# Optimization experiments

Hardware: AMD Instinct MI355X
Metric: run time of the kernel (lower is better)

The kernel has to match this reference:

```python
import jax, jax.numpy as jnp
import numpy as np

N_NODES = 50000
N_EDGES = 800000
D_IN = 128
D_OUT = 128
HEADS = 2
NEG_SLOPE = 0.2  # PyG GATConv default


def _gat_layer(x, src, dst, W, att_src, att_dst, bias):
    """One PyG-style GATConv with concat=False (mean over heads).
    x: [N, d_in], W: [d_in, H*d_out], att_src/att_dst: [H, d_out], bias: [d_out].
    Edge (j=src -> i=dst); softmax normalized over incoming edges of each dst node.
    """
    n = x.shape[0]
    d_out = att_src.shape[1]
    h = (x @ W).reshape(n, HEADS, d_out)                       # [N, H, D]
    a_s = jnp.einsum('nhd,hd->nh', h, att_src)                 # [N, H]
    a_d = jnp.einsum('nhd,hd->nh', h, att_dst)                 # [N, H]
    e = jax.nn.leaky_relu(a_s[src] + a_d[dst], NEG_SLOPE)      # [E, H]
    # numerically stable segment softmax over dst
    m = jax.ops.segment_max(e, dst, num_segments=n)            # [N, H]
    p = jnp.exp(e - m[dst])                                    # [E, H]
    s = jax.ops.segment_sum(p, dst, num_segments=n)            # [N, H]
    alpha = p / s[dst]                                         # [E, H]
    msg = h[src] * alpha[:, :, None]                           # [E, H, D]
    out = jax.ops.segment_sum(msg, dst, num_segments=n)        # [N, H, D]
    return out.mean(axis=1) + bias                             # concat=False -> mean heads


def setup_inputs() -> dict:
    key = jax.random.key(0)
    ks = jax.random.split(key, 10)
    sc = 0.05
    return {
        'x': jax.random.normal(ks[0], (N_NODES, D_IN), dtype=jnp.float32),
        'edge_index': jax.random.randint(ks[1], (2, N_EDGES), 0, N_NODES, dtype=jnp.int64),
        'W1': jax.random.normal(ks[2], (D_IN, HEADS * D_IN), dtype=jnp.float32) * sc,
        'att_src1': jax.random.normal(ks[3], (HEADS, D_IN), dtype=jnp.float32) * sc,
        'att_dst1': jax.random.normal(ks[4], (HEADS, D_IN), dtype=jnp.float32) * sc,
        'b1': jnp.zeros((D_IN,), dtype=jnp.float32),
        'W2': jax.random.normal(ks[5], (D_IN, HEADS * D_OUT), dtype=jnp.float32) * sc,
        'att_src2': jax.random.normal(ks[6], (HEADS, D_OUT), dtype=jnp.float32) * sc,
        'att_dst2': jax.random.normal(ks[7], (HEADS, D_OUT), dtype=jnp.float32) * sc,
        'b2': jnp.zeros((D_OUT,), dtype=jnp.float32),
    }


def reference(x, edge_index, W1, att_src1, att_dst1, b1, W2, att_src2, att_dst2, b2):
    n = x.shape[0]
    # PyG GATConv adds self-loops by default -> every node has >=1 incoming edge
    loops = jnp.arange(n, dtype=edge_index.dtype)
    src = jnp.concatenate([edge_index[0], loops])
    dst = jnp.concatenate([edge_index[1], loops])
    x = _gat_layer(x, src, dst, W1, att_src1, att_dst1, b1)
    x = _gat_layer(x, src, dst, W2, att_src2, att_dst2, b2)
    return x
```

## Files before the change

### kernel.cpp

```cpp
#include <hip/hip_runtime.h>
#include <hip/hip_bf16.h>

#define D 128
#define NCOLS 256
#define NPB 256
#define CAP 12288
#define P1CHUNK 4096

using f16x8 = __attribute__((ext_vector_type(8))) _Float16;
using f16x2 = __attribute__((ext_vector_type(2))) _Float16;
using f32x4 = __attribute__((ext_vector_type(4))) float;

__device__ inline int edge_val(const void* ei, int is32, long long idx) {
    if (is32) return ((const int*)ei)[idx];
    return (int)(((const long long*)ei)[idx]);
}

__global__ __launch_bounds__(256) void attprep_kernel(
    const float* __restrict__ W1, const float* __restrict__ as1,
    const float* __restrict__ ad1, float* __restrict__ v_s1,
    float* __restrict__ v_d1, _Float16* __restrict__ wT1,
    const float* __restrict__ W2, const float* __restrict__ as2,
    const float* __restrict__ ad2, float* __restrict__ v_s2,
    float* __restrict__ v_d2, _Float16* __restrict__ wT2,
    const void* __restrict__ ei, int* __restrict__ flag, int* __restrict__ gcnt) {
    int tid = threadIdx.x;
    if (blockIdx.x == 34) {
        gcnt[tid] = 0;
        if (tid == 0) *flag = 0;
        __syncthreads();
        const unsigned* u = (const unsigned*)ei;
        if (u[2 * tid + 1] != 0) *flag = 1;
        return;
    }
    int layer = blockIdx.x >= 17;
    int bx = blockIdx.x - (layer ? 17 : 0);
    const float* W = layer ? W2 : W1;
    const float* att_s = layer ? as2 : as1;
    const float* att_d = layer ? ad2 : ad1;
    float* v_s = layer ? v_s2 : v_s1;
    float* v_d = layer ? v_d2 : v_d1;
    _Float16* wT = layer ? wT2 : wT1;
    if (bx == 16) {
        int h = tid >> 7, d = tid & 127;
        const float* wrow = W + d * NCOLS + h * D;
        const float* as = att_s + h * D;
        const float* ad = att_d + h * D;
        float ss = 0.f, sd = 0.f;
        for (int i = 0; i < D; i += 4) {
            float4 wv = *reinterpret_cast<const float4*>(wrow + i);
            float4 av = *reinterpret_cast<const float4*>(as + i);
            float4 dv = *reinterpret_cast<const float4*>(ad + i);
            ss += wv.x * av.x + wv.y * av.y + wv.z * av.z + wv.w * av.w;
            sd += wv.x * dv.x + wv.y * dv.y + wv.z * dv.z + wv.w * dv.w;
        }
        v_s[tid] = ss;
        v_d[tid] = sd;
    } else {
        int base = bx * 2048 + tid * 8;
#pragma unroll
        for (int t = 0; t < 8; t += 4) {
            int f = base + t;
            int kk = f >> 7, i = f & 127;
            int h = kk >> 7, d = kk & 127;
            float4 wv = *reinterpret_cast<const float4*>(W + d * NCOLS + h * D + i);
            wT[(size_t)(i + 0) * NCOLS + kk] = (_Float16)(0.5f * wv.x);
            wT[(size_t)(i + 1) * NCOLS + kk] = (_Float16)(0.5f * wv.y);
            wT[(size_t)(i + 2) * NCOLS + kk] = (_Float16)(0.5f * wv.z);
            wT[(size_t)(i + 3) * NCOLS + kk] = (_Float16)(0.5f * wv.w);
        }
    }
}

__global__ __launch_bounds__(256) void bin_kernel(
    const void* __restrict__ ei, const int* __restrict__ flag,
    unsigned* __restrict__ bins, int* __restrict__ gcnt, int E, int nbuck) {
    __shared__ int cnt[256], cur[256], gb[256];
    int tid = threadIdx.x;
    int base = blockIdx.x * P1CHUNK;
    int m = min(P1CHUNK, E - base);
    int is32 = *flag;
    cnt[tid] = 0; cur[tid] = 0;
    __syncthreads();
    for (int i = tid; i < m; i += 256) {
        int dst = edge_val(ei, is32, (long long)E + base + i);
        atomicAdd(&cnt[dst >> 8], 1);
    }
    __syncthreads();
    if (tid < nbuck && cnt[tid] > 0) gb[tid] = atomicAdd(&gcnt[tid], cnt[tid]);
    else gb[tid] = 0;
    __syncthreads();
    for (int i = tid; i < m; i += 256) {
        int src = edge_val(ei, is32, base + i);
        int dst = edge_val(ei, is32, (long long)E + base + i);
        int b = dst >> 8;
        int pos = gb[b] + atomicAdd(&cur[b], 1);
        if (pos < CAP)
            bins[(size_t)b * CAP + pos] = ((unsigned)(dst & 255) << 16) | (unsigned)src;
    }
}

__global__ __launch_bounds__(256) void build_kernel(
    const unsigned* __restrict__ bins, const int* __restrict__ gcnt,
    int* __restrict__ row_ptr, int* __restrict__ csr_src, int n, int nbuck) {
    __shared__ unsigned items[CAP];
    __shared__ int deg[256], sc[256], cur[256], pref[256];
    int b = blockIdx.x, tid = threadIdx.x;
    int node0 = b * NPB;
    int nn = min(n - node0, NPB);
    int cnt = min(gcnt[b], CAP);
    int t = 0;
    if (tid < b) {
        int lo = tid * NPB, hi = min(n, lo + NPB);
        t = min(gcnt[tid], CAP) + (hi - lo);
    }
    pref[tid] = t;
    const unsigned* src = bins + (size_t)b * CAP;
    for (int i = tid; i < cnt; i += 256) items[i] = src[i];
    deg[tid] = (tid < nn) ? 1 : 0;
    __syncthreads();
#pragma unroll
    for (int off = 128; off >= 1; off >>= 1) {
        if (tid < off) pref[tid] += pref[tid + off];
        __syncthreads();
    }
    int gb = pref[0];
    for (int i = tid; i < cnt; i += 256) atomicAdd(&deg[(items[i] >> 16) & 255], 1);
    __syncthreads();
    int d = deg[tid];
    sc[tid] = d;
    __syncthreads();
#pragma unroll
    for (int off = 1; off < 256; off <<= 1) {
        int u = (tid >= off) ? sc[tid - off] : 0;
        __syncthreads();
        sc[tid] += u;
        __syncthreads();
    }
    int incl = sc[tid];
    int excl = incl - d;
    if (tid < nn) row_ptr[node0 + tid + 1] = gb + incl;
    if (b == 0 && tid == 0) row_ptr[0] = 0;
    cur[tid] = excl + ((tid < nn) ? 1 : 0);
    if (tid < nn) csr_src[gb + excl] = node0 + tid;
    __syncthreads();
    for (int i = tid; i < cnt; i += 256) {
        unsigned it = items[i];
        int p = atomicAdd(&cur[(it >> 16) & 255], 1);
        csr_src[gb + p] = (int)(it & 0xFFFFu);
    }
}

__global__ __launch_bounds__(256) void prep_x_kernel(
    const float* __restrict__ x, const float* __restrict__ v_s,
    const float* __restrict__ v_d, _Float16* __restrict__ xh,
    float* __restrict__ a_s, float* __restrict__ a_d, int n) {
    int lane = threadIdx.x & 63;
    int node = blockIdx.x * 4 + (threadIdx.x >> 6);
    if (node >= n) return;
    float2 xv = *reinterpret_cast<const float2*>(x + (size_t)node * D + 2 * lane);
    f16x2 hx = {(_Float16)xv.x, (_Float16)xv.y};
    *reinterpret_cast<f16x2*>(xh + (size_t)node * D + 2 * lane) = hx;
    float2 vs0 = *reinterpret_cast<const float2*>(v_s + 2 * lane);
    float2 vs1 = *reinterpret_cast<const float2*>(v_s + D + 2 * lane);
    float2 vd0 = *reinterpret_cast<const float2*>(v_d + 2 * lane);
    float2 vd1 = *reinterpret_cast<const float2*>(v_d + D + 2 * lane);
    float s0 = xv.x * vs0.x + xv.y * vs0.y;
    float s1 = xv.x * vs1.x + xv.y * vs1.y;
    float d0 = xv.x * vd0.x + xv.y * vd0.y;
    float d1 = xv.x * vd1.x + xv.y * vd1.y;
#pragma unroll
    for (int off = 1; off < 64; off <<= 1) {
        s0 += __shfl_xor(s0, off, 64);
        s1 += __shfl_xor(s1, off, 64);
        d0 += __shfl_xor(d0, off, 64);
        d1 += __shfl_xor(d1, off, 64);
    }
    if (lane == 0) {
        *reinterpret_cast<float2*>(a_s + (size_t)node * 2) = make_float2(s0, s1);
        *reinterpret_cast<float2*>(a_d + (size_t)node * 2) = make_float2(d0, d1);
    }
}

__global__ __launch_bounds__(256) void aggregate_kernel(
    const _Float16* __restrict__ xh, const float* __restrict__ a_s,
    const float* __restrict__ a_d, const int* __restrict__ row_ptr,
    const int* __restrict__ csr_src, _Float16* __restrict__ aggh, int n) {
    int lane = threadIdx.x & 63;
    int node = blockIdx.x * 4 + (threadIdx.x >> 6);
    if (node >= n) return;
    int beg = row_ptr[node], end = row_ptr[node + 1];
    float2 ad = *reinterpret_cast<const float2*>(a_d + (size_t)node * 2);
    int sub = lane >> 4, cq = lane & 15;
    float s0 = 0.f, s1 = 0.f;
    float acc0[8] = {}, acc1[8] = {};
    const _Float16* xb = xh + 8 * cq;
    for (int chunk = beg; chunk < end; chunk += 64) {
        int cnt = min(64, end - chunk);
        int j_l = 0;
        unsigned pp_l = 0;
        if (lane < cnt) {
            j_l = csr_src[chunk + lane];
            float2 as2 = *reinterpret_cast<const float2*>(a_s + (size_t)j_l * 2);
            float e0 = as2.x + ad.x; e0 = (e0 > 0.f) ? e0 : 0.2f * e0;
            float e1 = as2.y + ad.y; e1 = (e1 > 0.f) ? e1 : 0.2f * e1;
            f16x2 pq = {(_Float16)__expf(e0), (_Float16)__expf(e1)};
            pp_l = __builtin_bit_cast(unsigned, pq);
            s0 += (float)pq[0];
            s1 += (float)pq[1];
        }
#pragma unroll 4
        for (int k = 0; k < cnt; k += 4) {
            int idx = k + sub;
            unsigned ppu = (unsigned)__shfl((int)pp_l, idx, 64);
            int j = __shfl(j_l, idx, 64);
            f16x2 pq = __builtin_bit_cast(f16x2, ppu);
            float p0 = (float)pq[0], p1 = (float)pq[1];
            f16x8 hv = *reinterpret_cast<const f16x8*>(xb + (size_t)j * D);
#pragma unroll
            for (int i = 0; i < 8; ++i) {
                float h = (float)hv[i];
                acc0[i] += p0 * h;
                acc1[i] += p1 * h;
            }
        }
    }
#pragma unroll
    for (int i = 0; i < 8; ++i) {
        acc0[i] += __shfl_xor(acc0[i], 16, 64);
        acc0[i] += __shfl_xor(acc0[i], 32, 64);
        acc1[i] += __shfl_xor(acc1[i], 16, 64);
        acc1[i] += __shfl_xor(acc1[i], 32, 64);
    }
#pragma unroll
    for (int off = 1; off < 64; off <<= 1) {
        s0 += __shfl_xor(s0, off, 64);
        s1 += __shfl_xor(s1, off, 64);
    }
    if (sub == 0) {
        float i0 = 1.f / s0, i1 = 1.f / s1;
        f16x8 o0, o1;
#pragma unroll
        for (int i = 0; i < 8; ++i) {
            o0[i] = (_Float16)(acc0[i] * i0);
            o1[i] = (_Float16)(acc1[i] * i1);
        }
        *reinterpret_cast<f16x8*>(aggh + (size_t)node * NCOLS + 8 * cq)     = o0;
        *reinterpret_cast<f16x8*>(aggh + (size_t)node * NCOLS + D + 8 * cq) = o1;
    }
}

__global__ __launch_bounds__(256) void mfma_out_kernel(
    const _Float16* __restrict__ aggh, const _Float16* __restrict__ wT,
    const float* __restrict__ bias, const float* __restrict__ vs_next,
    const float* __restrict__ vd_next, float* __restrict__ as_next,
    float* __restrict__ ad_next, float* __restrict__ outf,
    _Float16* __restrict__ outh, int n) {
    int tid = threadIdx.x;
    int wave = tid >> 6, lane = tid & 63;
    int m0 = blockIdx.x * 64 + wave * 16;
    int ml = lane & 15;
    int g  = lane >> 4;
    int arow = m0 + ml; if (arow >= n) arow = n - 1;
    const _Float16* aA = aggh + (size_t)arow * NCOLS + 8 * g;
    const _Float16* bB = wT + (size_t)ml * NCOLS + 8 * g;

    f32x4 acc[8] = {};
#pragma unroll
    for (int kt = 0; kt < 8; ++kt) {
        int ko = kt * 32;
        f16x8 av = *reinterpret_cast<const f16x8*>(aA + ko);
#pragma unroll
        for (int nt = 0; nt < 8; ++nt) {
            f16x8 bv = *reinterpret_cast<const f16x8*>(bB + nt * 16 * NCOLS + ko);
            acc[nt] = __builtin_amdgcn_mfma_f32_16x16x32_f16(av, bv, acc[nt], 0, 0, 0);
        }
    }

    float bv8[8], vs0v[8], vs1v[8], vd0v[8], vd1v[8];
#pragma unroll
    for (int nt = 0; nt < 8; ++nt) bv8[nt] = bias[nt * 16 + ml];
    if (vs_next) {
#pragma unroll
        for (int nt = 0; nt < 8; ++nt) {
            int col = nt * 16 + ml;
            vs0v[nt] = vs_next[col];
            vs1v[nt] = vs_next[D + col];
            vd0v[nt] = vd_next[col];
            vd1v[nt] = vd_next[D + col];
        }
    }

#pragma unroll
    for (int r = 0; r < 4; ++r) {
        int orow = m0 + g * 4 + r;
        float vrow[8];
#pragma unroll
        for (int nt = 0; nt < 8; ++nt) vrow[nt] = acc[nt][r] + bv8[nt];
        if (orow < n) {
            if (outf) {
#pragma unroll
                for (int nt = 0; nt < 8; ++nt)
                    outf[(size_t)orow * D + nt * 16 + ml] = vrow[nt];
            }
            if (outh) {
#pragma unroll
                for (int nt = 0; nt < 8; ++nt)
                    outh[(size_t)orow * D + nt * 16 + ml] = (_Float16)vrow[nt];
            }
        }
        if (vs_next) {
            float ps0 = 0.f, ps1 = 0.f, pd0 = 0.f, pd1 = 0.f;
#pragma unroll
            for (int nt = 0; nt < 8; ++nt) {
                ps0 += vrow[nt] * vs0v[nt];
                ps1 += vrow[nt] * vs1v[nt];
                pd0 += vrow[nt] * vd0v[nt];
                pd1 += vrow[nt] * vd1v[nt];
            }
#pragma unroll
            for (int off = 1; off < 16; off <<= 1) {
                ps0 += __shfl_xor(ps0, off, 64);
                ps1 += __shfl_xor(ps1, off, 64);
                pd0 += __shfl_xor(pd0, off, 64);
                pd1 += __shfl_xor(pd1, off, 64);
            }
            if (ml == 0 && orow < n) {
                *reinterpret_cast<float2*>(as_next + (size_t)orow * 2) = make_float2(ps0, ps1);
                *reinterpret_cast<float2*>(ad_next + (size_t)orow * 2) = make_float2(pd0, pd1);
            }
        }
    }
}

extern "C" void kernel_launch(void* const* d_in, const int* in_sizes, int n_in,
                              void* d_out, int out_size, void* d_ws, size_t ws_size,
                              hipStream_t stream) {
    const float* x    = (const float*)d_in[0];
    const void*  ei   = d_in[1];
    const float* W1   = (const float*)d_in[2];
    const float* as1v = (const float*)d_in[3];
    const float* ad1v = (const float*)d_in[4];
    const float* b1   = (const float*)d_in[5];
    const float* W2   = (const float*)d_in[6];
    const float* as2v = (const float*)d_in[7];
    const float* ad2v = (const float*)d_in[8];
    const float* b2   = (const float*)d_in[9];
    float* out = (float*)d_out;

    const int N  = in_sizes[0] / D;
    const int E  = in_sizes[1] / 2;
    const int ET = E + N;
    const int NBUCK = (N + NPB - 1) / NPB;

    char* w = (char*)d_ws;
    size_t off = 0;
    auto alloc = [&](size_t bytes) {
        void* p = w + off;
        off = (off + bytes + 15) & ~(size_t)15;
        return p;
    };
    int*      flag    = (int*)     alloc(16);
    int*      gcnt    = (int*)     alloc(256 * 4);
    unsigned* bins    = (unsigned*)alloc((size_t)NBUCK * CAP * 4);
    int*      row_ptr = (int*)     alloc((size_t)(N + 1) * 4);
    int*      csr_src = (int*)     alloc((size_t)ET * 4);
    float*    v_s1    = (float*)   alloc(NCOLS * 4);
    float*    v_d1    = (float*)   alloc(NCOLS * 4);
    _Float16* wT1     = (_Float16*)alloc((size_t)NCOLS * D * 2);
    float*    v_s2    = (float*)   alloc(NCOLS * 4);
    float*    v_d2    = (float*)   alloc(NCOLS * 4);
    _Float16* wT2     = (_Float16*)alloc((size_t)NCOLS * D * 2);
    float*    a_s1    = (float*)   alloc((size_t)N * 2 * 4);
    float*    a_d1    = (float*)   alloc((size_t)N * 2 * 4);
    float*    a_s2    = (float*)   alloc((size_t)N * 2 * 4);
    float*    a_d2    = (float*)   alloc((size_t)N * 2 * 4);
    _Float16* xh      = (_Float16*)alloc((size_t)N * D * 2);
    _Float16* xmh     = (_Float16*)alloc((size_t)N * D * 2);
    _Float16* aggh    = (_Float16*)alloc((size_t)N * NCOLS * 2);

    hipLaunchKernelGGL(attprep_kernel, dim3(35), dim3(256), 0, stream,
                       W1, as1v, ad1v, v_s1, v_d1, wT1,
                       W2, as2v, ad2v, v_s2, v_d2, wT2, ei, flag, gcnt);
    hipLaunchKernelGGL(bin_kernel, dim3((E + P1CHUNK - 1) / P1CHUNK), dim3(256), 0, stream,
                       ei, flag, bins, gcnt, E, NBUCK);
    hipLaunchKernelGGL(build_kernel, dim3(NBUCK), dim3(256), 0, stream,
                       bins, gcnt, row_ptr, csr_src, N, NBUCK);

    hipLaunchKernelGGL(prep_x_kernel, dim3((N + 3) / 4), dim3(256), 0, stream,
                       x, v_s1, v_d1, xh, a_s1, a_d1, N);
    hipLaunchKernelGGL(aggregate_kernel, dim3((N + 3) / 4), dim3(256), 0, stream,
                       xh, a_s1, a_d1, row_ptr, csr_src, aggh, N);
    hipLaunchKernelGGL(mfma_out_kernel, dim3((N + 63) / 64), dim3(256), 0, stream,
                       aggh, wT1, b1, v_s2, v_d2, a_s2, a_d2,
                       (float*)nullptr, xmh, N);

    hipLaunchKernelGGL(aggregate_kernel, dim3((N + 3) / 4), dim3(256), 0, stream,
                       xmh, a_s2, a_d2, row_ptr, csr_src, aggh, N);
    hipLaunchKernelGGL(mfma_out_kernel, dim3((N + 63) / 64), dim3(256), 0, stream,
                       aggh, wT2, b2, (const float*)nullptr, (const float*)nullptr,
                       (float*)nullptr, (float*)nullptr, out, (_Float16*)nullptr, N);
}
```

Baseline: 217.4 us.

## Fuse aggregation with MFMA projection and merge binning with x prep

Each layer's gather-aggregate and MFMA output projection now run in one kernel. Each block aggregates 16 nodes into LDS in MFMA fragment layout, then multiplies by the transposed weight and reduces the next-layer attention scores through shared memory. This removes the N x 256 half-precision aggh round trip through global memory and one launch per layer. The edge binning and x fp16-prep kernels are merged into one launch by splitting the grid. The cost is that each wave now aggregates four nodes serially, which may lower latency hiding, and the new LDS reduction needs extra syncs.

```diff
diff --git a/kernel.cpp b/kernel.cpp
--- a/kernel.cpp
+++ b/kernel.cpp
@@ -72,31 +72,62 @@
     }
 }
 
-__global__ __launch_bounds__(256) void bin_kernel(
+__global__ __launch_bounds__(256) void binprep_kernel(
     const void* __restrict__ ei, const int* __restrict__ flag,
-    unsigned* __restrict__ bins, int* __restrict__ gcnt, int E, int nbuck) {
+    unsigned* __restrict__ bins, int* __restrict__ gcnt, int E, int nbuck,
+    const float* __restrict__ x, const float* __restrict__ v_s,
+    const float* __restrict__ v_d, _Float16* __restrict__ xh,
+    float* __restrict__ a_s, float* __restrict__ a_d, int n, int NBB) {
     __shared__ int cnt[256], cur[256], gb[256];
     int tid = threadIdx.x;
-    int base = blockIdx.x * P1CHUNK;
-    int m = min(P1CHUNK, E - base);
-    int is32 = *flag;
-    cnt[tid] = 0; cur[tid] = 0;
-    __syncthreads();
-    for (int i = tid; i < m; i += 256) {
-        int dst = edge_val(ei, is32, (long long)E + base + i);
-        atomicAdd(&cnt[dst >> 8], 1);
-    }
-    __syncthreads();
-    if (tid < nbuck && cnt[tid] > 0) gb[tid] = atomicAdd(&gcnt[tid], cnt[tid]);
-    else gb[tid] = 0;
-    __syncthreads();
-    for (int i = tid; i < m; i += 256) {
-        int src = edge_val(ei, is32, base + i);
-        int dst = edge_val(ei, is32, (long long)E + base + i);
-        int b = dst >> 8;
-        int pos = gb[b] + atomicAdd(&cur[b], 1);
-        if (pos < CAP)
-            bins[(size_t)b * CAP + pos] = ((unsigned)(dst & 255) << 16) | (unsigned)src;
+    if ((int)blockIdx.x < NBB) {
+        int base = blockIdx.x * P1CHUNK;
+        int m = min(P1CHUNK, E - base);
+        int is32 = *flag;
+        cnt[tid] = 0; cur[tid] = 0;
+        __syncthreads();
+        for (int i = tid; i < m; i += 256) {
+            int dst = edge_val(ei, is32, (long long)E + base + i);
+            atomicAdd(&cnt[dst >> 8], 1);
+        }
+        __syncthreads();
+        if (tid < nbuck && cnt[tid] > 0) gb[tid] = atomicAdd(&gcnt[tid], cnt[tid]);
+        else gb[tid] = 0;
+        __syncthreads();
+        for (int i = tid; i < m; i += 256) {
+            int src = edge_val(ei, is32, base + i);
+            int dst = edge_val(ei, is32, (long long)E + base + i);
+            int b = dst >> 8;
+            int pos = gb[b] + atomicAdd(&cur[b], 1);
+            if (pos < CAP)
+                bins[(size_t)b * CAP + pos] = ((unsigned)(dst & 255) << 16) | (unsigned)src;
+        }
+        return;
+    }
+    int lane = tid & 63;
+    int node = ((int)blockIdx.x - NBB) * 4 + (tid >> 6);
+    if (node >= n) return;
+    float2 xv = *reinterpret_cast<const float2*>(x + (size_t)node * D + 2 * lane);
+    f16x2 hx = {(_Float16)xv.x, (_Float16)xv.y};
+    *reinterpret_cast<f16x2*>(xh + (size_t)node * D + 2 * lane) = hx;
+    float2 vs0 = *reinterpret_cast<const float2*>(v_s + 2 * lane);
+    float2 vs1 = *reinterpret_cast<const float2*>(v_s + D + 2 * lane);
+    float2 vd0 = *reinterpret_cast<const float2*>(v_d + 2 * lane);
+    float2 vd1 = *reinterpret_cast<const float2*>(v_d + D + 2 * lane);
+    float s0 = xv.x * vs0.x + xv.y * vs0.y;
+    float s1 = xv.x * vs1.x + xv.y * vs1.y;
+    float d0 = xv.x * vd0.x + xv.y * vd0.y;
+    float d1 = xv.x * vd1.x + xv.y * vd1.y;
+#pragma unroll
+    for (int off = 1; off < 64; off <<= 1) {
+        s0 += __shfl_xor(s0, off, 64);
+        s1 += __shfl_xor(s1, off, 64);
+        d0 += __shfl_xor(d0, off, 64);
+        d1 += __shfl_xor(d1, off, 64);
+    }
+    if (lane == 0) {
+        *reinterpret_cast<float2*>(a_s + (size_t)node * 2) = make_float2(s0, s1);
+        *reinterpret_cast<float2*>(a_d + (size_t)node * 2) = make_float2(d0, d1);
     }
 }
 
@@ -151,173 +182,134 @@
     }
 }
 
-__global__ __launch_bounds__(256) void prep_x_kernel(
-    const float* __restrict__ x, const float* __restrict__ v_s,
-    const float* __restrict__ v_d, _Float16* __restrict__ xh,
-    float* __restrict__ a_s, float* __restrict__ a_d, int n) {
-    int lane = threadIdx.x & 63;
-    int node = blockIdx.x * 4 + (threadIdx.x >> 6);
-    if (node >= n) return;
-    float2 xv = *reinterpret_cast<const float2*>(x + (size_t)node * D + 2 * lane);
-    f16x2 hx = {(_Float16)xv.x, (_Float16)xv.y};
-    *reinterpret_cast<f16x2*>(xh + (size_t)node * D + 2 * lane) = hx;
-    float2 vs0 = *reinterpret_cast<const float2*>(v_s + 2 * lane);
-    float2 vs1 = *reinterpret_cast<const float2*>(v_s + D + 2 * lane);
-    float2 vd0 = *reinterpret_cast<const float2*>(v_d + 2 * lane);
-    float2 vd1 = *reinterpret_cast<const float2*>(v_d + D + 2 * lane);
-    float s0 = xv.x * vs0.x + xv.y * vs0.y;
-    float s1 = xv.x * vs1.x + xv.y * vs1.y;
-    float d0 = xv.x * vd0.x + xv.y * vd0.y;
-    float d1 = xv.x * vd1.x + xv.y * vd1.y;
-#pragma unroll
-    for (int off = 1; off < 64; off <<= 1) {
-        s0 += __shfl_xor(s0, off, 64);
-        s1 += __shfl_xor(s1, off, 64);
-        d0 += __shfl_xor(d0, off, 64);
-        d1 += __shfl_xor(d1, off, 64);
-    }
-    if (lane == 0) {
-        *reinterpret_cast<float2*>(a_s + (size_t)node * 2) = make_float2(s0, s1);
-        *reinterpret_cast<float2*>(a_d + (size_t)node * 2) = make_float2(d0, d1);
-    }
-}
-
-__global__ __launch_bounds__(256) void aggregate_kernel(
+__global__ __launch_bounds__(256) void agg_mfma_kernel(
     const _Float16* __restrict__ xh, const float* __restrict__ a_s,
     const float* __restrict__ a_d, const int* __restrict__ row_ptr,
-    const int* __restrict__ csr_src, _Float16* __restrict__ aggh, int n) {
-    int lane = threadIdx.x & 63;
-    int node = blockIdx.x * 4 + (threadIdx.x >> 6);
-    if (node >= n) return;
-    int beg = row_ptr[node], end = row_ptr[node + 1];
-    float2 ad = *reinterpret_cast<const float2*>(a_d + (size_t)node * 2);
-    int sub = lane >> 4, cq = lane & 15;
-    float s0 = 0.f, s1 = 0.f;
-    float acc0[8] = {}, acc1[8] = {};
-    const _Float16* xb = xh + 8 * cq;
-    for (int chunk = beg; chunk < end; chunk += 64) {
-        int cnt = min(64, end - chunk);
-        int j_l = 0;
-        unsigned pp_l = 0;
-        if (lane < cnt) {
-            j_l = csr_src[chunk + lane];
-            float2 as2 = *reinterpret_cast<const float2*>(a_s + (size_t)j_l * 2);
-            float e0 = as2.x + ad.x; e0 = (e0 > 0.f) ? e0 : 0.2f * e0;
-            float e1 = as2.y + ad.y; e1 = (e1 > 0.f) ? e1 : 0.2f * e1;
-            f16x2 pq = {(_Float16)__expf(e0), (_Float16)__expf(e1)};
-            pp_l = __builtin_bit_cast(unsigned, pq);
-            s0 += (float)pq[0];
-            s1 += (float)pq[1];
-        }
-#pragma unroll 4
-        for (int k = 0; k < cnt; k += 4) {
-            int idx = k + sub;
-            unsigned ppu = (unsigned)__shfl((int)pp_l, idx, 64);
-            int j = __shfl(j_l, idx, 64);
-            f16x2 pq = __builtin_bit_cast(f16x2, ppu);
-            float p0 = (float)pq[0], p1 = (float)pq[1];
-            f16x8 hv = *reinterpret_cast<const f16x8*>(xb + (size_t)j * D);
-#pragma unroll
-            for (int i = 0; i < 8; ++i) {
-                float h = (float)hv[i];
-                acc0[i] += p0 * h;
-                acc1[i] += p1 * h;
-            }
-        }
-    }
-#pragma unroll
-    for (int i = 0; i < 8; ++i) {
-        acc0[i] += __shfl_xor(acc0[i], 16, 64);
-        acc0[i] += __shfl_xor(acc0[i], 32, 64);
-        acc1[i] += __shfl_xor(acc1[i], 16, 64);
-        acc1[i] += __shfl_xor(acc1[i], 32, 64);
-    }
-#pragma unroll
-    for (int off = 1; off < 64; off <<= 1) {
-        s0 += __shfl_xor(s0, off, 64);
-        s1 += __shfl_xor(s1, off, 64);
-    }
-    if (sub == 0) {
-        float i0 = 1.f / s0, i1 = 1.f / s1;
-        f16x8 o0, o1;
-#pragma unroll
-        for (int i = 0; i < 8; ++i) {
-            o0[i] = (_Float16)(acc0[i] * i0);
-            o1[i] = (_Float16)(acc1[i] * i1);
-        }
-        *reinterpret_cast<f16x8*>(aggh + (size_t)node * NCOLS + 8 * cq)     = o0;
-        *reinterpret_cast<f16x8*>(aggh + (size_t)node * NCOLS + D + 8 * cq) = o1;
-    }
-}
-
-__global__ __launch_bounds__(256) void mfma_out_kernel(
-    const _Float16* __restrict__ aggh, const _Float16* __restrict__ wT,
+    const int* __restrict__ csr_src, const _Float16* __restrict__ wT,
     const float* __restrict__ bias, const float* __restrict__ vs_next,
     const float* __restrict__ vd_next, float* __restrict__ as_next,
     float* __restrict__ ad_next, float* __restrict__ outf,
     _Float16* __restrict__ outh, int n) {
+    __shared__ __align__(16) _Float16 Alds[8 * 512];
+    __shared__ float part[4][16][4];
     int tid = threadIdx.x;
     int wave = tid >> 6, lane = tid & 63;
-    int m0 = blockIdx.x * 64 + wave * 16;
-    int ml = lane & 15;
-    int g  = lane >> 4;
-    int arow = m0 + ml; if (arow >= n) arow = n - 1;
-    const _Float16* aA = aggh + (size_t)arow * NCOLS + 8 * g;
-    const _Float16* bB = wT + (size_t)ml * NCOLS + 8 * g;
-
-    f32x4 acc[8] = {};
+    int m0 = blockIdx.x * 16;
+    int sub = lane >> 4, cq = lane & 15;
+
+    const _Float16* xb = xh + 8 * cq;
+    for (int nd = 0; nd < 4; ++nd) {
+        int nl = wave * 4 + nd;
+        int node = m0 + nl;
+        if (node >= n) break;
+        int beg = row_ptr[node], end = row_ptr[node + 1];
+        float2 ad = *reinterpret_cast<const float2*>(a_d + (size_t)node * 2);
+        float s0 = 0.f, s1 = 0.f;
+        float acc0[8] = {}, acc1[8] = {};
+        for (int chunk = beg; chunk < end; chunk += 64) {
+            int cnt = min(64, end - chunk);
+            int j_l = 0;
+            unsigned pp_l = 0;
+            if (lane < cnt) {
+                j_l = csr_src[chunk + lane];
+                float2 as2 = *reinterpret_cast<const float2*>(a_s + (size_t)j_l * 2);
+                float e0 = as2.x + ad.x; e0 = (e0 > 0.f) ? e0 : 0.2f * e0;
+                float e1 = as2.y + ad.y; e1 = (e1 > 0.f) ? e1 : 0.2f * e1;
+                f16x2 pq = {(_Float16)__expf(e0), (_Float16)__expf(e1)};
+                pp_l = __builtin_bit_cast(unsigned, pq);
+                s0 += (float)pq[0];
+                s1 += (float)pq[1];
+            }
+#pragma unroll 4
+            for (int k = 0; k < cnt; k += 4) {
+                int idx = k + sub;
+                unsigned ppu = (unsigned)__shfl((int)pp_l, idx, 64);
+                int j = __shfl(j_l, idx, 64);
+                f16x2 pq = __builtin_bit_cast(f16x2, ppu);
+                float p0 = (float)pq[0], p1 = (float)pq[1];
+                f16x8 hv = *reinterpret_cast<const f16x8*>(xb + (size_t)j * D);
+#pragma unroll
+                for (int i = 0; i < 8; ++i) {
+                    float h = (float)hv[i];
+                    acc0[i] += p0 * h;
+                    acc1[i] += p1 * h;
+                }
+            }
+        }
+#pragma unroll
+        for (int i = 0; i < 8; ++i) {
+            acc0[i] += __shfl_xor(acc0[i], 16, 64);
+            acc0[i] += __shfl_xor(acc0[i], 32, 64);
+            acc1[i] += __shfl_xor(acc1[i], 16, 64);
+            acc1[i] += __shfl_xor(acc1[i], 32, 64);
+        }
+#pragma unroll
+        for (int off = 1; off < 64; off <<= 1) {
+            s0 += __shfl_xor(s0, off, 64);
+            s1 += __shfl_xor(s1, off, 64);
+        }
+        if (sub == 0) {
+            float i0 = 1.f / s0, i1 = 1.f / s1;
+            f16x8 o0, o1;
+#pragma unroll
+            for (int i = 0; i < 8; ++i) {
+                o0[i] = (_Float16)(acc0[i] * i0);
+                o1[i] = (_Float16)(acc1[i] * i1);
+            }
+            int kt0 = cq >> 2, g0 = cq & 3;
+            *reinterpret_cast<f16x8*>(Alds + kt0 * 512 + (g0 * 16 + nl) * 8)       = o0;
+            *reinterpret_cast<f16x8*>(Alds + (4 + kt0) * 512 + (g0 * 16 + nl) * 8) = o1;
+        }
+    }
+    __syncthreads();
+
+    int ml = lane & 15, g = lane >> 4;
+    f32x4 accA = {}, accB = {};
+    int nt0 = wave * 2, nt1 = wave * 2 + 1;
+    const _Float16* b0 = wT + (size_t)(nt0 * 16 + ml) * NCOLS + 8 * g;
+    const _Float16* b1 = wT + (size_t)(nt1 * 16 + ml) * NCOLS + 8 * g;
 #pragma unroll
     for (int kt = 0; kt < 8; ++kt) {
+        f16x8 av = *reinterpret_cast<const f16x8*>(Alds + kt * 512 + lane * 8);
         int ko = kt * 32;
-        f16x8 av = *reinterpret_cast<const f16x8*>(aA + ko);
-#pragma unroll
-        for (int nt = 0; nt < 8; ++nt) {
-            f16x8 bv = *reinterpret_cast<const f16x8*>(bB + nt * 16 * NCOLS + ko);
-            acc[nt] = __builtin_amdgcn_mfma_f32_16x16x32_f16(av, bv, acc[nt], 0, 0, 0);
-        }
-    }
-
-    float bv8[8], vs0v[8], vs1v[8], vd0v[8], vd1v[8];
-#pragma unroll
-    for (int nt = 0; nt < 8; ++nt) bv8[nt] = bias[nt * 16 + ml];
+        f16x8 bv0 = *reinterpret_cast<const f16x8*>(b0 + ko);
+        f16x8 bv1 = *reinterpret_cast<const f16x8*>(b1 + ko);
+        accA = __builtin_amdgcn_mfma_f32_16x16x32_f16(av, bv0, accA, 0, 0, 0);
+        accB = __builtin_amdgcn_mfma_f32_16x16x32_f16(av, bv1, accB, 0, 0, 0);
+    }
+
+    int col0 = nt0 * 16 + ml, col1 = nt1 * 16 + ml;
+    float bA = bias[col0], bB = bias[col1];
+    float vsA0 = 0.f, vsA1 = 0.f, vdA0 = 0.f, vdA1 = 0.f;
+    float vsB0 = 0.f, vsB1 = 0.f, vdB0 = 0.f, vdB1 = 0.f;
     if (vs_next) {
-#pragma unroll
-        for (int nt = 0; nt < 8; ++nt) {
-            int col = nt * 16 + ml;
-            vs0v[nt] = vs_next[col];
-            vs1v[nt] = vs_next[D + col];
-            vd0v[nt] = vd_next[col];
-            vd1v[nt] = vd_next[D + col];
-        }
+        vsA0 = vs_next[col0]; vsA1 = vs_next[D + col0];
+        vdA0 = vd_next[col0]; vdA1 = vd_next[D + col0];
+        vsB0 = vs_next[col1]; vsB1 = vs_next[D + col1];
+        vdB0 = vd_next[col1]; vdB1 = vd_next[D + col1];
     }
 
 #pragma unroll
     for (int r = 0; r < 4; ++r) {
-        int orow = m0 + g * 4 + r;
-        float vrow[8];
-#pragma unroll
-        for (int nt = 0; nt < 8; ++nt) vrow[nt] = acc[nt][r] + bv8[nt];
+        int lrow = g * 4 + r;
+        int orow = m0 + lrow;
+        float vA = accA[r] + bA;
+        float vB = accB[r] + bB;
         if (orow < n) {
             if (outf) {
-#pragma unroll
-                for (int nt = 0; nt < 8; ++nt)
-                    outf[(size_t)orow * D + nt * 16 + ml] = vrow[nt];
+                outf[(size_t)orow * D + col0] = vA;
+                outf[(size_t)orow * D + col1] = vB;
             }
             if (outh) {
-#pragma unroll
-                for (int nt = 0; nt < 8; ++nt)
-                    outh[(size_t)orow * D + nt * 16 + ml] = (_Float16)vrow[nt];
+                outh[(size_t)orow * D + col0] = (_Float16)vA;
+                outh[(size_t)orow * D + col1] = (_Float16)vB;
             }
         }
         if (vs_next) {
-            float ps0 = 0.f, ps1 = 0.f, pd0 = 0.f, pd1 = 0.f;
-#pragma unroll
-            for (int nt = 0; nt < 8; ++nt) {
-                ps0 += vrow[nt] * vs0v[nt];
-                ps1 += vrow[nt] * vs1v[nt];
-                pd0 += vrow[nt] * vd0v[nt];
-                pd1 += vrow[nt] * vd1v[nt];
-            }
+            float ps0 = vA * vsA0 + vB * vsB0;
+            float ps1 = vA * vsA1 + vB * vsB1;
+            float pd0 = vA * vdA0 + vB * vdB0;
+            float pd1 = vA * vdA1 + vB * vdB1;
 #pragma unroll
             for (int off = 1; off < 16; off <<= 1) {
                 ps0 += __shfl_xor(ps0, off, 64);
@@ -325,9 +317,24 @@
                 pd0 += __shfl_xor(pd0, off, 64);
                 pd1 += __shfl_xor(pd1, off, 64);
             }
-            if (ml == 0 && orow < n) {
-                *reinterpret_cast<float2*>(as_next + (size_t)orow * 2) = make_float2(ps0, ps1);
-                *reinterpret_cast<float2*>(ad_next + (size_t)orow * 2) = make_float2(pd0, pd1);
+            if (ml == 0) {
+                part[wave][lrow][0] = ps0;
+                part[wave][lrow][1] = ps1;
+                part[wave][lrow][2] = pd0;
+                part[wave][lrow][3] = pd1;
+            }
+        }
+    }
+    if (vs_next) {
+        __syncthreads();
+        if (tid < 64) {
+            int row = tid >> 2, q = tid & 3;
+            int node = m0 + row;
+            if (node < n) {
+                float v = part[0][row][q] + part[1][row][q]
+                        + part[2][row][q] + part[3][row][q];
+                float* dstp = (q < 2) ? as_next : ad_next;
+                dstp[(size_t)node * 2 + (q & 1)] = v;
             }
         }
     }
@@ -352,6 +359,7 @@
     const int E  = in_sizes[1] / 2;
     const int ET = E + N;
     const int NBUCK = (N + NPB - 1) / NPB;
+    const int NBB = (E + P1CHUNK - 1) / P1CHUNK;
 
     char* w = (char*)d_ws;
     size_t off = 0;
@@ -377,27 +385,20 @@
     float*    a_d2    = (float*)   alloc((size_t)N * 2 * 4);
     _Float16* xh      = (_Float16*)alloc((size_t)N * D * 2);
     _Float16* xmh     = (_Float16*)alloc((size_t)N * D * 2);
-    _Float16* aggh    = (_Float16*)alloc((size_t)N * NCOLS * 2);
 
     hipLaunchKernelGGL(attprep_kernel, dim3(35), dim3(256), 0, stream,
                        W1, as1v, ad1v, v_s1, v_d1, wT1,
                        W2, as2v, ad2v, v_s2, v_d2, wT2, ei, flag, gcnt);
-    hipLaunchKernelGGL(bin_kernel, dim3((E + P1CHUNK - 1) / P1CHUNK), dim3(256), 0, stream,
-                       ei, flag, bins, gcnt, E, NBUCK);
+    hipLaunchKernelGGL(binprep_kernel, dim3(NBB + (N + 3) / 4), dim3(256), 0, stream,
+                       ei, flag, bins, gcnt, E, NBUCK,
+                       x, v_s1, v_d1, xh, a_s1, a_d1, N, NBB);
     hipLaunchKernelGGL(build_kernel, dim3(NBUCK), dim3(256), 0, stream,
                        bins, gcnt, row_ptr, csr_src, N, NBUCK);
-
-    hipLaunchKernelGGL(prep_x_kernel, dim3((N + 3) / 4), dim3(256), 0, stream,
-                       x, v_s1, v_d1, xh, a_s1, a_d1, N);
-    hipLaunchKernelGGL(aggregate_kernel, dim3((N + 3) / 4), dim3(256), 0, stream,
-                       xh, a_s1, a_d1, row_ptr, csr_src, aggh, N);
-    hipLaunchKernelGGL(mfma_out_kernel, dim3((N + 63) / 64), dim3(256), 0, stream,
-                       aggh, wT1, b1, v_s2, v_d2, a_s2, a_d2,
-                       (float*)nullptr, xmh, N);
-
-    hipLaunchKernelGGL(aggregate_kernel, dim3((N + 3) / 4), dim3(256), 0, stream,
-                       xmh, a_s2, a_d2, row_ptr, csr_src, aggh, N);
-    hipLaunchKernelGGL(mfma_out_kernel, dim3((N + 63) / 64), dim3(256), 0, stream,
-                       aggh, wT2, b2, (const float*)nullptr, (const float*)nullptr,
+    hipLaunchKernelGGL(agg_mfma_kernel, dim3((N + 15) / 16), dim3(256), 0, stream,
+                       xh, a_s1, a_d1, row_ptr, csr_src, wT1, b1,
+                       v_s2, v_d2, a_s2, a_d2, (float*)nullptr, xmh, N);
+    hipLaunchKernelGGL(agg_mfma_kernel, dim3((N + 15) / 16), dim3(256), 0, stream,
+                       xmh, a_s2, a_d2, row_ptr, csr_src, wT2, b2,
+                       (const float*)nullptr, (const float*)nullptr,
                        (float*)nullptr, (float*)nullptr, out, (_Float16*)nullptr, N);
 }
```

New measurement: 179.2 us. 1.21x faster.
